# Optimization experiments

Hardware: AMD Instinct MI355X
Metric: run time of the kernel (lower is better)

## Reference

```python
import jax, jax.numpy as jnp
import numpy as np

B, N, D, E, F, K = 2, 2048, 768, 8, 3072, 2
V_MAX = 3.0
FEAT_CLAMP = 10.0


def setup_inputs() -> dict:
    key = jax.random.key(0)
    ks = jax.random.split(key, 8)
    s = lambda k, shape, sc: (jax.random.normal(k, shape, jnp.float32) * sc)
    return {
        "x": s(ks[0], (B, N, D), 1.0),
        "v_w": s(ks[1], (D,), 0.02),
        "v_b": jnp.zeros((), jnp.float32),
        "gate_w": s(ks[2], (D, E), 0.02),
        "gate_b": jnp.zeros((E,), jnp.float32),
        "w1": s(ks[3], (E, D, F), 0.02),
        "b1": jnp.zeros((E, F), jnp.float32),
        "w2": s(ks[4], (E, F, D), 0.02),
        "b2": jnp.zeros((E, D), jnp.float32),
        "out_w": s(ks[5], (2, D), 0.02),
        "out_b": jnp.zeros((D,), jnp.float32),
        "bk_scale": jnp.ones((D,), jnp.float32),
    }


def bk_green_diag(a):
    # a: (B, N) complex64 diagonal of (H_eps - z), unit off-diagonals.
    # Stable two-sided continued-fraction (Thomas/LDU) recursion:
    #   d_i = a_i - 1/d_{i-1},  e_i = a_i - 1/e_{i+1},  G_ii = 1/(d_i + e_i - a_i)
    aT = jnp.swapaxes(a, 0, 1)  # (N, B)

    def step(c, ai):
        d = ai - 1.0 / c
        return d, d

    d0 = aT[0]
    _, d_rest = jax.lax.scan(step, d0, aT[1:])
    d = jnp.concatenate([d0[None], d_rest], axis=0)  # (N, B)

    eN = aT[-1]
    _, e_rest = jax.lax.scan(step, eN, aT[:-1], reverse=True)
    e = jnp.concatenate([e_rest, eN[None]], axis=0)  # (N, B)

    G = 1.0 / (d + e - aT)
    return jnp.swapaxes(G, 0, 1)  # (B, N) complex


def reference(x, v_w, v_b, gate_w, gate_b, w1, b1, w2, b2, out_w, out_b, bk_scale):
    # --- potential projection: v = clamp(Linear(x), +-3) ---
    v = jnp.clip(x @ v_w + v_b, -V_MAX, V_MAX)  # (B, N)
    # H_eps diagonal = -2 + v, z = 1j  ->  A = H_eps - z
    a = ((-2.0 + v).astype(jnp.complex64) - 1j)
    G = bk_green_diag(a)  # (B, N) complex
    feats = jnp.stack([G.real, G.imag], axis=-1)  # (B, N, 2)

    # --- sparse MoE FFN (top-k softmax gating, GELU experts) ---
    logits = x @ gate_w + gate_b  # (B, N, E)
    probs = jax.nn.softmax(logits, axis=-1)
    topv, topi = jax.lax.top_k(probs, K)
    topv = topv / jnp.sum(topv, axis=-1, keepdims=True)
    comb = jnp.sum(topv[..., None] * jax.nn.one_hot(topi, E, dtype=x.dtype), axis=2)  # (B, N, E)
    h = jax.nn.gelu(jnp.einsum("bnd,edf->bnef", x, w1) + b1)  # (B, N, E, F)
    y = jnp.einsum("bnef,efd->bned", h, w2) + b2  # (B, N, E, D)
    ffn_out = jnp.einsum("bne,bned->bnd", comb, y)

    # --- spectral branch: clamp features, project to d_model, scale ---
    feats_c = jnp.clip(feats, -FEAT_CLAMP, FEAT_CLAMP)
    spec_out = feats_c @ out_w + out_b  # (B, N, D)
    return ffn_out + bk_scale * spec_out
```

## Files before the change

### kernel.cpp

```cpp
#include <hip/hip_runtime.h>
#include <hip/hip_bf16.h>

#define BB 2
#define NN 2048
#define DD 768
#define EE 8
#define FF 3072
#define TOK (BB*NN)
#define ROWS_CAP 9216
#define TILES 72

typedef __attribute__((ext_vector_type(8))) __bf16 bf16x8;
typedef __attribute__((ext_vector_type(4))) float floatx4;

#define OFF_CTRL    0ull
#define OFF_V       1024ull
#define OFF_TOKE    17408ull
#define OFF_TOKW    50176ull
#define OFF_ROWTOK  82944ull
#define OFF_ROWW    119808ull
#define OFF_SLOT    156672ull
#define OFF_FEATS   189440ull
#define OFF_W2T     222208ull
#define OFF_XBF     37970944ull
#define OFF_W1T     44262400ull
#define OFF_H       82011136ull
#define OFF_Y       OFF_XBF

__device__ __forceinline__ ushort f2b(float f) {
    union { float f; unsigned int i; } v; v.f = f;
    unsigned int u = v.i;
    unsigned int r = (u + 0x7FFFu + ((u >> 16) & 1u)) >> 16;
    return (ushort)r;
}
__device__ __forceinline__ unsigned int pk2(float lo, float hi) {
    union { float f; unsigned int u; } a, b;
    a.f = lo; b.f = hi;
    unsigned int ra = ((a.u + 0x7FFFu + ((a.u >> 16) & 1u)) >> 16) & 0xFFFFu;
    unsigned int rb = (b.u + 0x7FFFu + ((b.u >> 16) & 1u)) & 0xFFFF0000u;
    return ra | rb;
}
__device__ __forceinline__ float gelu_f(float x) {
    float z = 0.7978845608028654f * x * (1.f + 0.044715f * x * x);
    z = fminf(fmaxf(z, -12.f), 12.f);
    float e = __expf(2.f * z);
    return 0.5f * x * (1.f + (e - 1.f) / (e + 1.f));
}
__device__ __forceinline__ void gload16(const ushort* g, ushort* l) {
    __builtin_amdgcn_global_load_lds((const __attribute__((address_space(1))) void*)g,
                                     (__attribute__((address_space(3))) void*)l,
                                     16, 0, 0);
}

struct cplx { float x, y; };
__device__ __forceinline__ cplx cmulc(cplx a, cplx b) { return {a.x*b.x - a.y*b.y, a.x*b.y + a.y*b.x}; }
__device__ __forceinline__ cplx caddc(cplx a, cplx b) { return {a.x + b.x, a.y + b.y}; }
__device__ __forceinline__ cplx cdivc(cplx a, cplx b) {
    float s = 1.f / (b.x*b.x + b.y*b.y);
    return {(a.x*b.x + a.y*b.y)*s, (a.y*b.x - a.x*b.y)*s};
}
struct mob { cplx m00, m01, m10, m11; };
__device__ __forceinline__ mob mmul(const mob& A, const mob& B) {
    mob C;
    C.m00 = caddc(cmulc(A.m00, B.m00), cmulc(A.m01, B.m10));
    C.m01 = caddc(cmulc(A.m00, B.m01), cmulc(A.m01, B.m11));
    C.m10 = caddc(cmulc(A.m10, B.m00), cmulc(A.m11, B.m10));
    C.m11 = caddc(cmulc(A.m10, B.m01), cmulc(A.m11, B.m11));
    return C;
}
__device__ __forceinline__ void mnorm(mob& A) {
    float s = fabsf(A.m00.x);
    s = fmaxf(s, fabsf(A.m00.y)); s = fmaxf(s, fabsf(A.m01.x)); s = fmaxf(s, fabsf(A.m01.y));
    s = fmaxf(s, fabsf(A.m10.x)); s = fmaxf(s, fabsf(A.m10.y)); s = fmaxf(s, fabsf(A.m11.x));
    s = fmaxf(s, fabsf(A.m11.y));
    float r = 1.f / fmaxf(s, 1e-30f);
    A.m00.x *= r; A.m00.y *= r; A.m01.x *= r; A.m01.y *= r;
    A.m10.x *= r; A.m10.y *= r; A.m11.x *= r; A.m11.y *= r;
}
__device__ __forceinline__ mob mstep(cplx a, const mob& P) {
    mob C;
    C.m00 = {a.x*P.m00.x - a.y*P.m00.y - P.m10.x, a.x*P.m00.y + a.y*P.m00.x - P.m10.y};
    C.m01 = {a.x*P.m01.x - a.y*P.m01.y - P.m11.x, a.x*P.m01.y + a.y*P.m01.x - P.m11.y};
    C.m10 = P.m00; C.m11 = P.m01;
    return C;
}
__device__ __forceinline__ void mstore(float* s, const mob& A) {
    s[0]=A.m00.x; s[1]=A.m00.y; s[2]=A.m01.x; s[3]=A.m01.y;
    s[4]=A.m10.x; s[5]=A.m10.y; s[6]=A.m11.x; s[7]=A.m11.y;
}
__device__ __forceinline__ mob mload(const float* s) {
    mob A;
    A.m00 = {s[0], s[1]}; A.m01 = {s[2], s[3]};
    A.m10 = {s[4], s[5]}; A.m11 = {s[6], s[7]};
    return A;
}

#define NB_CVT   ((TOK*DD)/8/256)
#define NB_ROUTE (TOK/4)
#define NB_T1    ((FF/128)*(DD/32)*EE)
#define NB_T2    ((DD/128)*(FF/32)*EE)

__device__ __forceinline__ void cvt_body(const float* __restrict__ src, ushort* __restrict__ dst, int i) {
    const float4* s = ((const float4*)src) + (size_t)i * 2;
    float4 a = s[0], b = s[1];
    uint4 o;
    o.x = pk2(a.x, a.y); o.y = pk2(a.z, a.w);
    o.z = pk2(b.x, b.y); o.w = pk2(b.z, b.w);
    *(((uint4*)dst) + i) = o;
}

__device__ __forceinline__ void tcvt4_body(const float* __restrict__ src, ushort* __restrict__ dst,
                                           int R, int C, int bx, int by, int bz,
                                           float (*t)[33]) {
    size_t eoff = (size_t)bz * R * C;
    const float* s = src + eoff;
    ushort* d = dst + eoff;
    int c0 = bx * 128, r0 = by * 32;
    int tid = threadIdx.x;
    int tr = tid >> 3, tc = (tid & 7) * 4;
    float4 v[4];
    const float* srow = s + (size_t)(r0 + tr) * C + c0 + tc;
    #pragma unroll
    for (int k = 0; k < 4; k++) v[k] = *(const float4*)(srow + k * 32);
    #pragma unroll
    for (int k = 0; k < 4; k++) {
        __syncthreads();
        t[tr][tc] = v[k].x; t[tr][tc+1] = v[k].y; t[tr][tc+2] = v[k].z; t[tr][tc+3] = v[k].w;
        __syncthreads();
        ushort4 o;
        o.x = f2b(t[tc  ][tr]);
        o.y = f2b(t[tc+1][tr]);
        o.z = f2b(t[tc+2][tr]);
        o.w = f2b(t[tc+3][tr]);
        *(ushort4*)(d + (size_t)(c0 + k*32 + tr) * R + r0 + tc) = o;
    }
}

__device__ __forceinline__ void routing_body(
    const float* __restrict__ x, const float* __restrict__ v_w, const float* __restrict__ v_b,
    const float* __restrict__ gate_w, const float* __restrict__ gate_b,
    float* __restrict__ v_out, int* __restrict__ tok_e, float* __restrict__ tok_w, int blk)
{
    int wave = threadIdx.x >> 6, lane = threadIdx.x & 63;
    int t = blk * 4 + wave;
    const float* xr = x + (size_t)t * DD;
    float av = 0.f;
    float ag[8] = {0.f, 0.f, 0.f, 0.f, 0.f, 0.f, 0.f, 0.f};
    #pragma unroll
    for (int i = 0; i < 12; i++) {
        int d = lane + 64 * i;
        float xv = xr[d];
        av += xv * v_w[d];
        const float4* g = (const float4*)(gate_w + d * 8);
        float4 g0 = g[0], g1 = g[1];
        ag[0] += xv * g0.x; ag[1] += xv * g0.y; ag[2] += xv * g0.z; ag[3] += xv * g0.w;
        ag[4] += xv * g1.x; ag[5] += xv * g1.y; ag[6] += xv * g1.z; ag[7] += xv * g1.w;
    }
    #pragma unroll
    for (int off = 32; off >= 1; off >>= 1) {
        av += __shfl_xor(av, off);
        #pragma unroll
        for (int e = 0; e < 8; e++) ag[e] += __shfl_xor(ag[e], off);
    }
    if (lane == 0) {
        float vv = av + v_b[0];
        vv = fminf(fmaxf(vv, -3.f), 3.f);
        v_out[t] = vv;
        float lg[8];
        #pragma unroll
        for (int e = 0; e < 8; e++) lg[e] = ag[e] + gate_b[e];
        int e0 = 0;
        #pragma unroll
        for (int e = 1; e < 8; e++) if (lg[e] > lg[e0]) e0 = e;
        int e1 = -1;
        #pragma unroll
        for (int e = 0; e < 8; e++) if (e != e0 && (e1 < 0 || lg[e] > lg[e1])) e1 = e;
        float w0 = 1.f / (1.f + __expf(lg[e1] - lg[e0]));
        tok_e[2*t] = e0; tok_e[2*t+1] = e1;
        tok_w[2*t] = w0; tok_w[2*t+1] = 1.f - w0;
    }
}

__global__ __launch_bounds__(256) void prep_kernel(
    const float* __restrict__ x, ushort* __restrict__ x_bf,
    const float* __restrict__ v_w, const float* __restrict__ v_b,
    const float* __restrict__ gate_w, const float* __restrict__ gate_b,
    float* __restrict__ v_out, int* __restrict__ tok_e, float* __restrict__ tok_w,
    const float* __restrict__ w1, ushort* __restrict__ w1t,
    const float* __restrict__ w2, ushort* __restrict__ w2t)
{
    __shared__ float t[32][33];
    int id = blockIdx.x;
    if (id < NB_CVT) {
        cvt_body(x, x_bf, id * 256 + threadIdx.x);
        return;
    }
    id -= NB_CVT;
    if (id < NB_ROUTE) {
        routing_body(x, v_w, v_b, gate_w, gate_b, v_out, tok_e, tok_w, id);
        return;
    }
    id -= NB_ROUTE;
    if (id < NB_T1) {
        int bx = id % (FF/128); int by = (id / (FF/128)) % (DD/32); int bz = id / ((FF/128)*(DD/32));
        tcvt4_body(w1, w1t, DD, FF, bx, by, bz, t);
        return;
    }
    id -= NB_T1;
    {
        int bx = id % (DD/128); int by = (id / (DD/128)) % (FF/32); int bz = id / ((DD/128)*(FF/32));
        tcvt4_body(w2, w2t, FF, DD, bx, by, bz, t);
    }
}

__device__ void setup_body(
    const int* __restrict__ tok_e, const float* __restrict__ tok_w,
    int* __restrict__ ctrl, int* __restrict__ row_token, float* __restrict__ row_w,
    int* __restrict__ slot)
{
    __shared__ int cnt[8], base[8], cursor[8];
    int tid = threadIdx.x;
    int lane = tid & 63;
    if (tid < 8) { cnt[tid] = 0; cursor[tid] = 0; }
    __syncthreads();

    int mye[8];
    #pragma unroll
    for (int it = 0; it < 8; it++) {
        int idx = it * 1024 + tid;
        int e = tok_e[idx];
        mye[it] = e;
        #pragma unroll
        for (int ex = 0; ex < 8; ex++) {
            unsigned long long m = __ballot(e == ex);
            if (e == ex && lane == (__ffsll((long long)m) - 1))
                atomicAdd(&cnt[ex], (int)__popcll(m));
        }
    }
    __syncthreads();
    if (tid == 0) {
        int b = 0;
        int* te = ctrl + 24;
        for (int i = 0; i < TILES; i++) te[i] = -1;
        #pragma unroll
        for (int e = 0; e < EE; e++) {
            base[e] = b;
            ctrl[16 + e] = b;
            int tiles = (cnt[e] + 127) >> 7;
            int t0 = b >> 7;
            for (int i = 0; i < tiles; i++) te[t0 + i] = e;
            b += tiles << 7;
        }
    }
    for (int p = tid; p < ROWS_CAP; p += 1024) row_token[p] = -1;
    __syncthreads();

    #pragma unroll
    for (int it = 0; it < 8; it++) {
        int idx = it * 1024 + tid;
        int e = mye[it];
        unsigned long long lt = (1ull << lane) - 1ull;
        int p = 0;
        #pragma unroll
        for (int ex = 0; ex < 8; ex++) {
            unsigned long long m = __ballot(e == ex);
            if (e == ex) {
                int leader = __ffsll((long long)m) - 1;
                int pos = (int)__popcll(m & lt);
                int bp = 0;
                if (lane == leader) bp = atomicAdd(&cursor[ex], (int)__popcll(m));
                bp = __shfl(bp, leader);
                p = base[ex] + bp + pos;
            }
        }
        row_token[p] = idx >> 1;
        row_w[p] = tok_w[idx];
        slot[idx] = p;
    }
}

__device__ void bk_body(int b, const float* __restrict__ v, float* __restrict__ feats) {
    int t = threadIdx.x;
    bool act = t < 256;
    __shared__ float sm[256][8];
    const mob I = {{1.f,0.f},{0.f,0.f},{0.f,0.f},{1.f,0.f}};
    cplx a[8];
    const float* vb = v + (size_t)b * NN;
    if (act) {
        #pragma unroll
        for (int j = 0; j < 8; j++) { a[j].x = -2.f + vb[t*8 + j]; a[j].y = -1.f; }
    }

    mob cur = I;
    if (act) {
        #pragma unroll
        for (int j = 0; j < 8; j++) cur = mstep(a[j], cur);
        mnorm(cur);
        mstore(sm[t], cur);
    }
    for (int s = 1; s < 256; s <<= 1) {
        __syncthreads();
        mob prev; bool has = act && (t >= s);
        if (has) prev = mload(sm[t - s]);
        __syncthreads();
        if (has) { cur = mmul(cur, prev); mnorm(cur); mstore(sm[t], cur); }
    }
    __syncthreads();
    cplx dreg[8];
    if (act) {
        mob P = (t > 0) ? mload(sm[t - 1]) : I;
        #pragma unroll
        for (int j = 0; j < 8; j++) {
            P = mstep(a[j], P); mnorm(P);
            dreg[j] = cdivc(P.m00, P.m10);
        }
    }
    __syncthreads();

    cur = I;
    if (act) {
        #pragma unroll
        for (int j = 7; j >= 0; j--) cur = mstep(a[j], cur);
        mnorm(cur);
        mstore(sm[t], cur);
    }
    for (int s = 1; s < 256; s <<= 1) {
        __syncthreads();
        mob nxt; bool has = act && (t + s < 256);
        if (has) nxt = mload(sm[t + s]);
        __syncthreads();
        if (has) { cur = mmul(cur, nxt); mnorm(cur); mstore(sm[t], cur); }
    }
    __syncthreads();
    if (act) {
        mob P = (t < 255) ? mload(sm[t + 1]) : I;
        #pragma unroll
        for (int j = 7; j >= 0; j--) {
            P = mstep(a[j], P); mnorm(P);
            cplx e = cdivc(P.m00, P.m10);
            cplx den = {dreg[j].x + e.x - a[j].x, dreg[j].y + e.y - a[j].y};
            cplx one = {1.f, 0.f};
            cplx G = cdivc(one, den);
            int i = b * NN + t*8 + j;
            feats[2*i]   = G.x;
            feats[2*i+1] = G.y;
        }
    }
}

__global__ __launch_bounds__(1024) void setup_bk_kernel(
    const int* __restrict__ tok_e, const float* __restrict__ tok_w,
    int* __restrict__ ctrl, int* __restrict__ row_token, float* __restrict__ row_w,
    int* __restrict__ slot, const float* __restrict__ v, float* __restrict__ feats)
{
    if (blockIdx.x == 0) setup_body(tok_e, tok_w, ctrl, row_token, row_w, slot);
    else                 bk_body(blockIdx.x - 1, v, feats);
}

#define MFMAS() do { \
        _Pragma("unroll") \
        for (int i = 0; i < 4; i++) \
            _Pragma("unroll") \
            for (int j = 0; j < 4; j++) \
                acc[i][j] = __builtin_amdgcn_mfma_f32_16x16x32_bf16(afr[i], bfr[j], acc[i][j], 0, 0, 0); \
    } while (0)

__global__ __launch_bounds__(512, 4) void gemm1_kernel(
    const ushort* __restrict__ x_bf, const ushort* __restrict__ w1t, const float* __restrict__ b1,
    const int* __restrict__ ctrl, const int* __restrict__ row_token, ushort* __restrict__ H)
{
    int tile = blockIdx.y;
    int e0 = ctrl[24 + 2*tile];
    if (e0 < 0) return;
    int e1 = ctrl[24 + 2*tile + 1];
    if (e1 < 0) e1 = e0;
    int p0 = tile * 256;
    int f0 = blockIdx.x * 128;

    __shared__ ushort As[2][256 * 32];
    __shared__ ushort Bs[2][256 * 32];
    __shared__ int toks[256];

    int tid = threadIdx.x;
    if (tid < 256) { int tk = row_token[p0 + tid]; toks[tid] = tk < 0 ? 0 : tk; }
    __syncthreads();

    int wave = tid >> 6, lane = tid & 63;
    int rsub = lane >> 2;
    int kq = (((lane & 3) ^ ((rsub >> 1) & 3))) * 8;
    int tokA0 = toks[wave*32 + rsub];
    int tokA1 = toks[wave*32 + 16 + rsub];
    const ushort* aglob0 = x_bf + (size_t)tokA0 * DD + kq;
    const ushort* aglob1 = x_bf + (size_t)tokA1 * DD + kq;
    int eh = (wave >> 2) ? e1 : e0;
    const ushort* w1e = w1t + (size_t)eh * (FF * DD);
    const ushort* bglob0 = w1e + (size_t)(f0 + (wave & 3)*32 + rsub) * DD + kq;
    const ushort* bglob1 = bglob0 + (size_t)16 * DD;
    ushort* AsW0 = &As[0][wave * 32 * 32];
    ushort* BsW0 = &Bs[0][wave * 32 * 32];
    ushort* AsW1 = &As[1][wave * 32 * 32];
    ushort* BsW1 = &Bs[1][wave * 32 * 32];

    floatx4 zero4 = {0.f, 0.f, 0.f, 0.f};
    floatx4 acc[4][4];
    #pragma unroll
    for (int i = 0; i < 4; i++)
        #pragma unroll
        for (int j = 0; j < 4; j++) acc[i][j] = zero4;

    int wm = (wave >> 1) * 64, wn = (wave & 1) * 64;
    int bbase = (wave >> 2) * 128;
    int lm = lane & 15, q = lane >> 4;
    int qx = (q ^ ((lm >> 1) & 3)) * 8;

    #define G1_STAGE(AW, BW, k0) do { \
        gload16(aglob0 + (k0), (AW)); \
        gload16(aglob1 + (k0), (AW) + 16*32); \
        gload16(bglob0 + (k0), (BW)); \
        gload16(bglob1 + (k0), (BW) + 16*32); } while (0)

    G1_STAGE(AsW0, BsW0, 0);
    G1_STAGE(AsW1, BsW1, 32);
    const int NK = DD / 32;
    for (int ks = 0; ks < NK; ks++) {
        int cur = ks & 1;
        const ushort* Ab = cur ? As[1] : As[0];
        const ushort* Bb = cur ? Bs[1] : Bs[0];
        ushort* AsN = cur ? AsW1 : AsW0;
        ushort* BsN = cur ? BsW1 : BsW0;
        if (ks < NK - 1) { asm volatile("s_waitcnt vmcnt(4)" ::: "memory"); }
        else             { asm volatile("s_waitcnt vmcnt(0)" ::: "memory"); }
        __builtin_amdgcn_s_barrier();
        bf16x8 afr[4], bfr[4];
        #pragma unroll
        for (int i = 0; i < 4; i++)
            afr[i] = *(const bf16x8*)(const void*)(Ab + (wm + i*16 + lm) * 32 + qx);
        #pragma unroll
        for (int j = 0; j < 4; j++)
            bfr[j] = *(const bf16x8*)(const void*)(Bb + (bbase + wn + j*16 + lm) * 32 + qx);
        asm volatile("s_waitcnt lgkmcnt(0)" ::: "memory");
        __builtin_amdgcn_sched_barrier(0);
        __builtin_amdgcn_s_barrier();
        if (ks + 2 < NK) G1_STAGE(AsN, BsN, ks*32 + 64);
        __builtin_amdgcn_s_setprio(1);
        MFMAS();
        __builtin_amdgcn_s_setprio(0);
    }
    #undef G1_STAGE

    #pragma unroll
    for (int i = 0; i < 4; i++) {
        #pragma unroll
        for (int j = 0; j < 4; j++) {
            int n = wn + j*16 + lm;
            float bias = b1[eh * FF + f0 + n];
            #pragma unroll
            for (int r = 0; r < 4; r++) {
                int m = wm + i*16 + q*4 + r;
                float hv = gelu_f(acc[i][j][r] + bias);
                H[(size_t)(p0 + m) * FF + f0 + n] = f2b(hv);
            }
        }
    }
}

#define STAGE64(AW, BW, k0) do { \
        _Pragma("unroll") \
        for (int g = 0; g < 4; g++) { \
            gload16(ag[g] + (k0), (AW) + g*8*64); \
            gload16(bg[g] + (k0), (BW) + g*8*64); \
        } } while (0)

#define LOADFR64(APTR, BPTR, QX) do { \
        _Pragma("unroll") \
        for (int i = 0; i < 4; i++) \
            afr[i] = *(const bf16x8*)(const void*)((APTR) + (wm + i*16 + lm) * 64 + (QX)); \
        _Pragma("unroll") \
        for (int j = 0; j < 4; j++) \
            bfr[j] = *(const bf16x8*)(const void*)((BPTR) + (wn + j*16 + lm) * 64 + (QX)); \
    } while (0)

#define PIPE64(NK) do { \
    STAGE64(AsW0, BsW0, 0); \
    STAGE64(AsW1, BsW1, 64); \
    for (int ks = 0; ks < (NK); ks++) { \
        int cur = ks & 1; \
        const ushort* Ab = cur ? As[1] : As[0]; \
        const ushort* Bb = cur ? Bs[1] : Bs[0]; \
        ushort* AsN = cur ? AsW1 : AsW0; \
        ushort* BsN = cur ? BsW1 : BsW0; \
        if (ks < (NK) - 1) { asm volatile("s_waitcnt vmcnt(8)" ::: "memory"); } \
        else               { asm volatile("s_waitcnt vmcnt(0)" ::: "memory"); } \
        __builtin_amdgcn_s_barrier(); \
        { \
            bf16x8 afr[4], bfr[4]; \
            LOADFR64(Ab, Bb, qx0); \
            __builtin_amdgcn_s_setprio(1); \
            MFMAS(); \
            __builtin_amdgcn_s_setprio(0); \
        } \
        { \
            bf16x8 afr[4], bfr[4]; \
            LOADFR64(Ab, Bb, qx0 ^ 32); \
            asm volatile("s_waitcnt lgkmcnt(0)" ::: "memory"); \
            __builtin_amdgcn_sched_barrier(0); \
            __builtin_amdgcn_s_barrier(); \
            if (ks + 2 < (NK)) STAGE64(AsN, BsN, ks*64 + 128); \
            __builtin_amdgcn_s_setprio(1); \
            MFMAS(); \
            __builtin_amdgcn_s_setprio(0); \
        } \
    } } while (0)

__global__ __launch_bounds__(256) void gemm2_kernel(
    const ushort* __restrict__ H, const ushort* __restrict__ w2t, const float* __restrict__ b2,
    const int* __restrict__ ctrl, const float* __restrict__ row_w, float* __restrict__ Y)
{
    int tile = blockIdx.x;
    int e = ctrl[24 + tile];
    if (e < 0) return;
    int p0 = tile * 128;
    int d0 = blockIdx.y * 128;

    __shared__ ushort As[2][128 * 64];
    __shared__ ushort Bs[2][128 * 64];

    int tid = threadIdx.x;
    int wave = tid >> 6, lane = tid & 63;
    int srow = lane >> 3;
    int kq = (((lane & 7) ^ (srow & 7))) * 8;
    const ushort* ag[4];
    #pragma unroll
    for (int g = 0; g < 4; g++)
        ag[g] = H + (size_t)(p0 + wave*32 + g*8 + srow) * FF + kq;
    const ushort* w2e = w2t + (size_t)e * (DD * FF);
    const ushort* bg[4];
    #pragma unroll
    for (int g = 0; g < 4; g++)
        bg[g] = w2e + (size_t)(d0 + wave*32 + g*8 + srow) * FF + kq;
    ushort* AsW0 = &As[0][wave * 32 * 64];
    ushort* BsW0 = &Bs[0][wave * 32 * 64];
    ushort* AsW1 = &As[1][wave * 32 * 64];
    ushort* BsW1 = &Bs[1][wave * 32 * 64];

    floatx4 zero4 = {0.f, 0.f, 0.f, 0.f};
    floatx4 acc[4][4];
    #pragma unroll
    for (int i = 0; i < 4; i++)
        #pragma unroll
        for (int j = 0; j < 4; j++) acc[i][j] = zero4;

    int wm = (wave & 1) * 64, wn = (wave >> 1) * 64;
    int lm = lane & 15, q = lane >> 4;
    int qx0 = (q ^ (lm & 7)) * 8;

    PIPE64(FF/64);

    #pragma unroll
    for (int i = 0; i < 4; i++) {
        #pragma unroll
        for (int j = 0; j < 4; j++) {
            int n = wn + j*16 + lm;
            float bias = b2[e * DD + d0 + n];
            #pragma unroll
            for (int r = 0; r < 4; r++) {
                int m = wm + i*16 + q*4 + r;
                float wgt = row_w[p0 + m];
                Y[(size_t)(p0 + m) * DD + d0 + n] = wgt * (acc[i][j][r] + bias);
            }
        }
    }
}

__global__ __launch_bounds__(256) void final_kernel(
    const float* __restrict__ Y, const int* __restrict__ slot, const float* __restrict__ feats,
    const float* __restrict__ out_w, const float* __restrict__ out_b,
    const float* __restrict__ bk_scale, float* __restrict__ out)
{
    int idx = blockIdx.x * 256 + threadIdx.x;
    int base = idx * 4;
    int t = base / DD;
    int d = base - t * DD;
    int p0 = slot[2*t], p1 = slot[2*t + 1];
    const float4 ya = *(const float4*)(Y + (size_t)p0 * DD + d);
    const float4 yb = *(const float4*)(Y + (size_t)p1 * DD + d);
    float f0 = feats[2*t], f1 = feats[2*t + 1];
    f0 = fminf(fmaxf(f0, -10.f), 10.f);
    f1 = fminf(fmaxf(f1, -10.f), 10.f);
    float ff[4] = {ya.x + yb.x, ya.y + yb.y, ya.z + yb.z, ya.w + yb.w};
    float4 o;
    float* op = (float*)&o;
    #pragma unroll
    for (int u = 0; u < 4; u++) {
        float spec = f0 * out_w[d + u] + f1 * out_w[DD + d + u] + out_b[d + u];
        op[u] = ff[u] + bk_scale[d + u] * spec;
    }
    *(float4*)(out + base) = o;
}

extern "C" void kernel_launch(void* const* d_in, const int* in_sizes, int n_in,
                              void* d_out, int out_size, void* d_ws, size_t ws_size,
                              hipStream_t stream)
{
    const float* x      = (const float*)d_in[0];
    const float* v_w    = (const float*)d_in[1];
    const float* v_b    = (const float*)d_in[2];
    const float* gate_w = (const float*)d_in[3];
    const float* gate_b = (const float*)d_in[4];
    const float* w1     = (const float*)d_in[5];
    const float* b1     = (const float*)d_in[6];
    const float* w2     = (const float*)d_in[7];
    const float* b2     = (const float*)d_in[8];
    const float* out_w  = (const float*)d_in[9];
    const float* out_b  = (const float*)d_in[10];
    const float* bk_s   = (const float*)d_in[11];

    char* ws = (char*)d_ws;
    int*    ctrl    = (int*)(ws + OFF_CTRL);
    float*  v       = (float*)(ws + OFF_V);
    int*    tok_e   = (int*)(ws + OFF_TOKE);
    float*  tok_w   = (float*)(ws + OFF_TOKW);
    int*    row_tok = (int*)(ws + OFF_ROWTOK);
    float*  row_w   = (float*)(ws + OFF_ROWW);
    int*    slot    = (int*)(ws + OFF_SLOT);
    float*  feats   = (float*)(ws + OFF_FEATS);
    ushort* w2t     = (ushort*)(ws + OFF_W2T);
    ushort* x_bf    = (ushort*)(ws + OFF_XBF);
    ushort* w1t     = (ushort*)(ws + OFF_W1T);
    ushort* H       = (ushort*)(ws + OFF_H);
    float*  Y       = (float*)(ws + OFF_Y);
    float*  out     = (float*)d_out;

    prep_kernel<<<NB_CVT + NB_ROUTE + NB_T1 + NB_T2, 256, 0, stream>>>(
        x, x_bf, v_w, v_b, gate_w, gate_b, v, tok_e, tok_w, w1, w1t, w2, w2t);
    setup_bk_kernel<<<1 + BB, 1024, 0, stream>>>(tok_e, tok_w, ctrl, row_tok, row_w, slot, v, feats);
    gemm1_kernel<<<dim3(FF / 128, TILES / 2), 512, 0, stream>>>(x_bf, w1t, b1, ctrl, row_tok, H);
    gemm2_kernel<<<dim3(TILES, DD / 128), 256, 0, stream>>>(H, w2t, b2, ctrl, row_w, Y);
    final_kernel<<<(TOK * DD) / 1024, 256, 0, stream>>>(Y, slot, feats, out_w, out_b, bk_s, out);
}
```

Measured before the change: 208.4 us.

## Move w2 transpose into gemm1 launch and use 64x64 bf16 transpose tiles

Replaces the 32x33 float-tile transpose with a 64x64 tile that converts to bf16 before staging in shared memory and writes 16-byte rows. The w2 transpose moves out of the prep kernel and runs as extra blocks appended to the gemm1 grid, so it can overlap with gemm1 instead of delaying setup. Its output uses a permuted k order that gemm2 presumably expects. The gemm1 epilogue also packs two bf16 outputs per 32-bit store. The risk is that the extra blocks compete with gemm1 for CUs, and that the permutation must match what gemm2 reads.

```diff
diff --git a/kernel.cpp b/kernel.cpp
--- a/kernel.cpp
+++ b/kernel.cpp
@@ -95,10 +95,51 @@
     return A;
 }
 
+template<bool PERM>
+__device__ __forceinline__ void tcvt64_body(
+    const float* __restrict__ src, ushort* __restrict__ dst,
+    int Rs, int Cs, int r0, int c0, ushort* __restrict__ tT , int tid)
+{
+    int lr = tid >> 2;
+    int lc0 = (tid & 3) * 16;
+    const float* sp = src + (size_t)(r0 + lr) * Cs + c0 + lc0;
+    float4 v[4];
+    #pragma unroll
+    for (int u = 0; u < 4; u++) v[u] = *(const float4*)(sp + 4*u);
+    #pragma unroll
+    for (int u = 0; u < 4; u++) {
+        tT[(lc0 + 4*u + 0) * 72 + lr] = f2b(v[u].x);
+        tT[(lc0 + 4*u + 1) * 72 + lr] = f2b(v[u].y);
+        tT[(lc0 + 4*u + 2) * 72 + lr] = f2b(v[u].z);
+        tT[(lc0 + 4*u + 3) * 72 + lr] = f2b(v[u].w);
+    }
+    __syncthreads();
+    int chunk = tid & 7;
+    #pragma unroll
+    for (int pass = 0; pass < 2; pass++) {
+        int c = (tid >> 3) + pass * 32;
+        size_t off = (size_t)(c0 + c) * Rs + r0 + chunk * 8;
+        if (PERM) {
+            int a64 = chunk * 8;
+            int g32 = (a64 >> 5) * 32;
+            int a = a64 & 31;
+            ushort o8[8] __attribute__((aligned(16)));
+            #pragma unroll
+            for (int k = 0; k < 8; k++) {
+                int pk = a + k;
+                int rl = g32 + (pk >> 1) + ((pk & 1) << 4);
+                o8[k] = tT[c * 72 + rl];
+            }
+            *(uint4*)(dst + off) = *(const uint4*)o8;
+        } else {
+            *(uint4*)(dst + off) = *(const uint4*)(tT + c * 72 + chunk * 8);
+        }
+    }
+}
+
 #define NB_CVT   ((TOK*DD)/8/256)
 #define NB_ROUTE (TOK/4)
-#define NB_T1    ((FF/128)*(DD/32)*EE)
-#define NB_T2    ((DD/128)*(FF/32)*EE)
+#define NB_W1T   (12*48*EE)
 
 __device__ __forceinline__ void cvt_body(const float* __restrict__ src, ushort* __restrict__ dst, int i) {
     const float4* s = ((const float4*)src) + (size_t)i * 2;
@@ -107,33 +148,6 @@
     o.x = pk2(a.x, a.y); o.y = pk2(a.z, a.w);
     o.z = pk2(b.x, b.y); o.w = pk2(b.z, b.w);
     *(((uint4*)dst) + i) = o;
-}
-
-__device__ __forceinline__ void tcvt4_body(const float* __restrict__ src, ushort* __restrict__ dst,
-                                           int R, int C, int bx, int by, int bz,
-                                           float (*t)[33]) {
-    size_t eoff = (size_t)bz * R * C;
-    const float* s = src + eoff;
-    ushort* d = dst + eoff;
-    int c0 = bx * 128, r0 = by * 32;
-    int tid = threadIdx.x;
-    int tr = tid >> 3, tc = (tid & 7) * 4;
-    float4 v[4];
-    const float* srow = s + (size_t)(r0 + tr) * C + c0 + tc;
-    #pragma unroll
-    for (int k = 0; k < 4; k++) v[k] = *(const float4*)(srow + k * 32);
-    #pragma unroll
-    for (int k = 0; k < 4; k++) {
-        __syncthreads();
-        t[tr][tc] = v[k].x; t[tr][tc+1] = v[k].y; t[tr][tc+2] = v[k].z; t[tr][tc+3] = v[k].w;
-        __syncthreads();
-        ushort4 o;
-        o.x = f2b(t[tc  ][tr]);
-        o.y = f2b(t[tc+1][tr]);
-        o.z = f2b(t[tc+2][tr]);
-        o.w = f2b(t[tc+3][tr]);
-        *(ushort4*)(d + (size_t)(c0 + k*32 + tr) * R + r0 + tc) = o;
-    }
 }
 
 __device__ __forceinline__ void routing_body(
@@ -181,15 +195,14 @@
     }
 }
 
-__global__ __launch_bounds__(256) void prep_kernel(
+__global__ __launch_bounds__(256) void prep1_kernel(
     const float* __restrict__ x, ushort* __restrict__ x_bf,
     const float* __restrict__ v_w, const float* __restrict__ v_b,
     const float* __restrict__ gate_w, const float* __restrict__ gate_b,
     float* __restrict__ v_out, int* __restrict__ tok_e, float* __restrict__ tok_w,
-    const float* __restrict__ w1, ushort* __restrict__ w1t,
-    const float* __restrict__ w2, ushort* __restrict__ w2t)
-{
-    __shared__ float t[32][33];
+    const float* __restrict__ w1, ushort* __restrict__ w1t)
+{
+    __shared__ __align__(16) ushort tT[64 * 72];
     int id = blockIdx.x;
     if (id < NB_CVT) {
         cvt_body(x, x_bf, id * 256 + threadIdx.x);
@@ -201,16 +214,12 @@
         return;
     }
     id -= NB_ROUTE;
-    if (id < NB_T1) {
-        int bx = id % (FF/128); int by = (id / (FF/128)) % (DD/32); int bz = id / ((FF/128)*(DD/32));
-        tcvt4_body(w1, w1t, DD, FF, bx, by, bz, t);
-        return;
-    }
-    id -= NB_T1;
-    {
-        int bx = id % (DD/128); int by = (id / (DD/128)) % (FF/32); int bz = id / ((DD/128)*(FF/32));
-        tcvt4_body(w2, w2t, FF, DD, bx, by, bz, t);
-    }
+    int e = id / (12 * 48);
+    int rem = id - e * 12 * 48;
+    int cy = rem / 12;
+    int rx = rem - cy * 12;
+    tcvt64_body<false>(w1 + (size_t)e * DD * FF, w1t + (size_t)e * FF * DD,
+                       DD, FF, rx * 64, cy * 64, tT, threadIdx.x);
 }
 
 __device__ void setup_body(
@@ -365,23 +374,45 @@
                 acc[i][j] = __builtin_amdgcn_mfma_f32_16x16x32_bf16(afr[i], bfr[j], acc[i][j], 0, 0, 0); \
     } while (0)
 
-__global__ __launch_bounds__(512, 4) void gemm1_kernel(
+#define G1N   (24 * 36)
+#define NW2T  (48 * 12 * EE / 2)
+
+__global__ __launch_bounds__(512, 4) void gemm1_fused_kernel(
     const ushort* __restrict__ x_bf, const ushort* __restrict__ w1t, const float* __restrict__ b1,
-    const int* __restrict__ ctrl, const int* __restrict__ row_token, ushort* __restrict__ H)
-{
-    int tile = blockIdx.y;
+    const int* __restrict__ ctrl, const int* __restrict__ row_token, ushort* __restrict__ H,
+    const float* __restrict__ w2, ushort* __restrict__ w2t)
+{
+    __shared__ __align__(16) ushort SH[4][256 * 32];
+    __shared__ int toks[256];
+    int bid = blockIdx.x;
+    int tid = threadIdx.x;
+
+    if (bid >= G1N) {
+        int tt = (bid - G1N) * 2 + (tid >> 8);
+        int e = tt / (48 * 12);
+        int rem = tt - e * 48 * 12;
+        int cy = rem / 48;
+        int rx = rem - cy * 48;
+        ushort* tT = &SH[0][0] + (tid >> 8) * 4608;
+        tcvt64_body<true>(w2 + (size_t)e * FF * DD, w2t + (size_t)e * DD * FF,
+                          FF, DD, rx * 64, cy * 64, tT, tid & 255);
+        return;
+    }
+
+    int fx = bid % 24;
+    int tile = bid / 24;
     int e0 = ctrl[24 + 2*tile];
     if (e0 < 0) return;
     int e1 = ctrl[24 + 2*tile + 1];
     if (e1 < 0) e1 = e0;
     int p0 = tile * 256;
-    int f0 = blockIdx.x * 128;
-
-    __shared__ ushort As[2][256 * 32];
-    __shared__ ushort Bs[2][256 * 32];
-    __shared__ int toks[256];
-
-    int tid = threadIdx.x;
+    int f0 = fx * 128;
+
+    ushort* As0 = &SH[0][0];
+    ushort* As1 = &SH[1][0];
+    ushort* Bs0 = &SH[2][0];
+    ushort* Bs1 = &SH[3][0];
+
     if (tid < 256) { int tk = row_token[p0 + tid]; toks[tid] = tk < 0 ? 0 : tk; }
     __syncthreads();
 
@@ -396,10 +427,10 @@
     const ushort* w1e = w1t + (size_t)eh * (FF * DD);
     const ushort* bglob0 = w1e + (size_t)(f0 + (wave & 3)*32 + rsub) * DD + kq;
     const ushort* bglob1 = bglob0 + (size_t)16 * DD;
-    ushort* AsW0 = &As[0][wave * 32 * 32];
-    ushort* BsW0 = &Bs[0][wave * 32 * 32];
-    ushort* AsW1 = &As[1][wave * 32 * 32];
-    ushort* BsW1 = &Bs[1][wave * 32 * 32];
+    ushort* AsW0 = As0 + wave * 32 * 32;
+    ushort* BsW0 = Bs0 + wave * 32 * 32;
+    ushort* AsW1 = As1 + wave * 32 * 32;
+    ushort* BsW1 = Bs1 + wave * 32 * 32;
 
     floatx4 zero4 = {0.f, 0.f, 0.f, 0.f};
     floatx4 acc[4][4];
@@ -424,8 +455,8 @@
     const int NK = DD / 32;
     for (int ks = 0; ks < NK; ks++) {
         int cur = ks & 1;
-        const ushort* Ab = cur ? As[1] : As[0];
-        const ushort* Bb = cur ? Bs[1] : Bs[0];
+        const ushort* Ab = cur ? As1 : As0;
+        const ushort* Bb = cur ? Bs1 : Bs0;
         ushort* AsN = cur ? AsW1 : AsW0;
         ushort* BsN = cur ? BsW1 : BsW0;
         if (ks < NK - 1) { asm volatile("s_waitcnt vmcnt(4)" ::: "memory"); }
@@ -451,14 +482,15 @@
     #pragma unroll
     for (int i = 0; i < 4; i++) {
         #pragma unroll
-        for (int j = 0; j < 4; j++) {
-            int n = wn + j*16 + lm;
-            float bias = b1[eh * FF + f0 + n];
+        for (int jp = 0; jp < 2; jp++) {
+            float bias0 = b1[eh * FF + f0 + wn + (2*jp)*16 + lm];
+            float bias1 = b1[eh * FF + f0 + wn + (2*jp+1)*16 + lm];
             #pragma unroll
             for (int r = 0; r < 4; r++) {
                 int m = wm + i*16 + q*4 + r;
-                float hv = gelu_f(acc[i][j][r] + bias);
-                H[(size_t)(p0 + m) * FF + f0 + n] = f2b(hv);
+                float h0 = gelu_f(acc[i][2*jp][r] + bias0);
+                float h1 = gelu_f(acc[i][2*jp+1][r] + bias1);
+                *(unsigned int*)(H + (size_t)(p0 + m) * FF + f0 + wn + jp*32 + lm*2) = pk2(h0, h1);
             }
         }
     }
@@ -631,10 +663,10 @@
     float*  Y       = (float*)(ws + OFF_Y);
     float*  out     = (float*)d_out;
 
-    prep_kernel<<<NB_CVT + NB_ROUTE + NB_T1 + NB_T2, 256, 0, stream>>>(
-        x, x_bf, v_w, v_b, gate_w, gate_b, v, tok_e, tok_w, w1, w1t, w2, w2t);
+    prep1_kernel<<<NB_CVT + NB_ROUTE + NB_W1T, 256, 0, stream>>>(
+        x, x_bf, v_w, v_b, gate_w, gate_b, v, tok_e, tok_w, w1, w1t);
     setup_bk_kernel<<<1 + BB, 1024, 0, stream>>>(tok_e, tok_w, ctrl, row_tok, row_w, slot, v, feats);
-    gemm1_kernel<<<dim3(FF / 128, TILES / 2), 512, 0, stream>>>(x_bf, w1t, b1, ctrl, row_tok, H);
+    gemm1_fused_kernel<<<G1N + NW2T, 512, 0, stream>>>(x_bf, w1t, b1, ctrl, row_tok, H, w2, w2t);
     gemm2_kernel<<<dim3(TILES, DD / 128), 256, 0, stream>>>(H, w2t, b2, ctrl, row_w, Y);
     final_kernel<<<(TOK * DD) / 1024, 256, 0, stream>>>(Y, slot, feats, out_w, out_b, bk_s, out);
 }
```

Result: faster. 197.8 us (-5.1%).
